# Optimization experiments

Measured on AMD Instinct MI355X. Metric: run time of the kernel, lower is better.

Reference implementation:

```python
import jax, jax.numpy as jnp
import numpy as np
import math

B, S, E, H = 4, 1024, 1024, 16
HD = E // H
MAX_SEQ = 5000
THETA = 10000.0


def _freqs_cis():
    # RotaryPositionalEncoding buffer: complex64 [MAX_SEQ, E//2]
    freqs = 1.0 / (THETA ** (np.arange(0, E, 2)[: E // 2] / E))
    ang = np.outer(np.arange(MAX_SEQ), freqs)
    return jnp.asarray(np.exp(1j * ang).astype(np.complex64))


def _rope(x, idx, fc_table):
    # x: [B, S, E]; pairs consecutive channels across the FULL embed_dim
    # (applied before head splitting, faithful to the original module)
    xc = x.reshape(*x.shape[:-1], -1, 2)
    xc = jax.lax.complex(xc[..., 0], xc[..., 1])  # [B, S, E//2]
    out = xc * fc_table[idx]                       # [B, S, E//2]
    return jnp.stack([jnp.real(out), jnp.imag(out)], axis=-1).reshape(x.shape)


def reference(query, key, value, query_index, key_index, attn_mask,
              key_padding_mask, Wq, bq, Wk, bk, Wv, bv, Wo, bo):
    q = query @ Wq.T + bq
    k = key @ Wk.T + bk
    v = value @ Wv.T + bv

    fc = _freqs_cis()
    q = _rope(q, query_index, fc)
    k = _rope(k, key_index, fc)

    # torch: q = cat(q.chunk(H, dim=-1), dim=0) -> flat HEAD-MAJOR [H*B, S, HD]
    qf = q.reshape(B, S, H, HD).transpose(2, 0, 1, 3).reshape(H * B, S, HD)
    kf = k.reshape(B, S, H, HD).transpose(2, 0, 1, 3).reshape(H * B, S, HD)
    vf = v.reshape(B, S, H, HD).transpose(2, 0, 1, 3).reshape(H * B, S, HD)

    # mask: logical_or(attn_mask[Sq,Sk], kpm[B,1,Sk]) -> [B, Sq, Sk]
    m = jnp.logical_or(attn_mask[None, :, :], key_padding_mask[:, None, :])
    madd = jnp.where(m, -jnp.inf, 0.0).astype(query.dtype)
    # torch repeat_interleave(H, dim=0) yields BATCH-MAJOR flat [B*H, Sq, Sk];
    # it is added to the head-major scores as-is (faithful to the original
    # indexing, including its head/batch-order quirk)
    madd_flat = jnp.repeat(madd, H, axis=0)

    scores = jnp.einsum('nqd,nkd->nqk', qf / math.sqrt(HD), kf) + madd_flat
    w = jax.nn.softmax(scores, axis=-1)              # [H*B, Sq, Sk]
    of = jnp.einsum('nqk,nkd->nqd', w, vf)           # [H*B, Sq, HD]

    # cat(chunks(dim=0), dim=-1) -> [B, Sq, E], head-major last dim
    attn_output = of.reshape(H, B, S, HD).transpose(1, 2, 0, 3).reshape(B, S, E)
    attn_output = attn_output @ Wo.T + bo

    # stack(chunks(dim=0), dim=1).mean(1) -> [B, Sq, Sk]
    attn_weights = w.reshape(H, B, S, S).transpose(1, 0, 2, 3).mean(axis=1)
    return attn_output, attn_weights


def setup_inputs() -> dict:
    key0 = jax.random.key(0)
    ks = jax.random.split(key0, 10)
    sc = 0.02
    inp = {
        'query': jax.random.normal(ks[0], (B, S, E), jnp.float32),
        'key': jax.random.normal(ks[1], (B, S, E), jnp.float32),
        'value': jax.random.normal(ks[2], (B, S, E), jnp.float32),
        'query_index': jnp.sort(jax.random.randint(ks[3], (B, S), 0, 4096), axis=-1),
        'key_index': jnp.sort(jax.random.randint(ks[4], (B, S), 0, 4096), axis=-1),
        'attn_mask': jnp.triu(jnp.ones((S, S), jnp.bool_), k=1),  # causal
        'key_padding_mask': jnp.zeros((B, S), jnp.bool_),
        'Wq': jax.random.normal(ks[5], (E, E), jnp.float32) * sc,
        'bq': jnp.zeros((E,), jnp.float32),
        'Wk': jax.random.normal(ks[6], (E, E), jnp.float32) * sc,
        'bk': jnp.zeros((E,), jnp.float32),
        'Wv': jax.random.normal(ks[7], (E, E), jnp.float32) * sc,
        'bv': jnp.zeros((E,), jnp.float32),
        'Wo': jax.random.normal(ks[8], (E, E), jnp.float32) * sc,
        'bo': jnp.zeros((E,), jnp.float32),
    }
    return inp
```

## Files before the change

kernel.cpp:

```cpp
#include <hip/hip_runtime.h>
#include <stdint.h>
#include <math.h>

#define B_ 4
#define S_ 1024
#define E_ 1024
#define H_ 16
#define HD_ 64
#define HB_ 64

typedef __attribute__((ext_vector_type(8))) short bhalf8;
typedef __attribute__((ext_vector_type(4))) float floatx4;

__device__ __forceinline__ unsigned short f2bf(float f) {
  union { float f; unsigned u; } v; v.f = f;
  unsigned r = (v.u + 0x7FFFu + ((v.u >> 16) & 1u)) >> 16;
  return (unsigned short)r;
}
__device__ __forceinline__ float bf2f(unsigned short b) {
  union { unsigned u; float f; } v; v.u = ((unsigned)b) << 16;
  return v.f;
}
__device__ __forceinline__ unsigned cvtpk_bf16(float a, float b) {
  unsigned r;
  asm volatile("v_cvt_pk_bf16_f32 %0, %1, %2" : "=v"(r) : "v"(a), "v"(b));
  return r;
}

__device__ __forceinline__ void gload16(const void* g, void* l) {
  __builtin_amdgcn_global_load_lds(
      (const __attribute__((address_space(1))) unsigned int*)g,
      (__attribute__((address_space(3))) unsigned int*)l, 16, 0, 0);
}

template <int NCH>
__device__ __forceinline__ void stage_tile(const unsigned short* org,
                                           unsigned short* lds, int wave, int lane) {
  const int rl = lane >> 3;
  const int scb = ((lane & 7) << 4) ^ (rl << 4);
  const char* base = (const char*)org + scb;
#pragma unroll
  for (int i = 0; i < NCH / 4; ++i) {
    const int c = wave + 4 * i;
    gload16(base + (size_t)(c * 8 + rl) * 2048, (char*)lds + c * 1024);
  }
}

__device__ __forceinline__ bhalf8 read_frag(const unsigned short* lds, int row, int kbyte) {
  const int off = row * 128 + (kbyte ^ ((row & 7) << 4));
  return *(const bhalf8*)((const char*)lds + off);
}

__global__ void detect_bool_kernel(const uint8_t* __restrict__ amask, int* __restrict__ flag) {
  if (threadIdx.x == 0 && blockIdx.x == 0) *flag = (amask[1] != 0) ? 1 : 0;
}

__global__ __launch_bounds__(256) void mprep_kernel(
    const void* __restrict__ amask, const void* __restrict__ kpm,
    const int* __restrict__ flagp, unsigned long long* __restrict__ Mbits) {
  const int gid = blockIdx.x * 256 + threadIdx.x;
  const int word = gid & 15, q = (gid >> 4) & 1023, bp = gid >> 14;
  const int k0 = word * 64;
  unsigned long long bits = 0;
  if (*flagp) {
    const uint8_t* ap = (const uint8_t*)amask + (size_t)q * 1024 + k0;
    const uint8_t* kp = (const uint8_t*)kpm + (size_t)bp * 1024 + k0;
#pragma unroll
    for (int c = 0; c < 4; ++c) {
      uint4 a = *(const uint4*)(ap + c * 16);
      uint4 k = *(const uint4*)(kp + c * 16);
      unsigned aw[4] = {a.x | k.x, a.y | k.y, a.z | k.z, a.w | k.w};
#pragma unroll
      for (int wv = 0; wv < 4; ++wv)
#pragma unroll
        for (int bt = 0; bt < 4; ++bt)
          if ((aw[wv] >> (8 * bt)) & 0xffu)
            bits |= 1ull << (c * 16 + wv * 4 + bt);
    }
  } else {
    const int* ap = (const int*)amask + (size_t)q * 1024 + k0;
    const int* kp = (const int*)kpm + (size_t)bp * 1024 + k0;
#pragma unroll
    for (int c = 0; c < 16; ++c) {
      int4 a = *(const int4*)(ap + c * 4);
      int4 k = *(const int4*)(kp + c * 4);
      if (a.x | k.x) bits |= 1ull << (c * 4 + 0);
      if (a.y | k.y) bits |= 1ull << (c * 4 + 1);
      if (a.z | k.z) bits |= 1ull << (c * 4 + 2);
      if (a.w | k.w) bits |= 1ull << (c * 4 + 3);
    }
  }
  Mbits[((size_t)bp << 14) + (size_t)q * 16 + word] = bits;
}

__global__ __launch_bounds__(256) void cvt_in_kernel(
    const float* __restrict__ q, const float* __restrict__ k,
    const float* __restrict__ v, unsigned short* __restrict__ Ab) {
  const int z = blockIdx.z;
  const float* src = (z == 0) ? q : (z == 1) ? k : v;
  unsigned short* dst = Ab + (size_t)z * 4194304;
  const size_t i = ((size_t)blockIdx.x * 256 + threadIdx.x) * 8;
  float4 a = *(const float4*)(src + i);
  float4 b = *(const float4*)(src + i + 4);
  bhalf8 r;
  r[0] = (short)f2bf(a.x); r[1] = (short)f2bf(a.y);
  r[2] = (short)f2bf(a.z); r[3] = (short)f2bf(a.w);
  r[4] = (short)f2bf(b.x); r[5] = (short)f2bf(b.y);
  r[6] = (short)f2bf(b.z); r[7] = (short)f2bf(b.w);
  *(bhalf8*)(dst + i) = r;
}

__global__ __launch_bounds__(256) void cvt_w_kernel(
    const float* __restrict__ wq, const float* __restrict__ wk,
    const float* __restrict__ wv, const float* __restrict__ wo,
    unsigned short* __restrict__ Wb) {
  const int z = blockIdx.z;
  const float* src = (z == 0) ? wq : (z == 1) ? wk : (z == 2) ? wv : wo;
  unsigned short* dst = Wb + (size_t)z * 1048576;
  const size_t i = ((size_t)blockIdx.x * 256 + threadIdx.x) * 8;
  float4 a = *(const float4*)(src + i);
  float4 b = *(const float4*)(src + i + 4);
  bhalf8 r;
  r[0] = (short)f2bf(a.x); r[1] = (short)f2bf(a.y);
  r[2] = (short)f2bf(a.z); r[3] = (short)f2bf(a.w);
  r[4] = (short)f2bf(b.x); r[5] = (short)f2bf(b.y);
  r[6] = (short)f2bf(b.z); r[7] = (short)f2bf(b.w);
  *(bhalf8*)(dst + i) = r;
}

template <bool BF16OUT>
__global__ __launch_bounds__(256) void mfma_gemm_kernel(
    const unsigned short* __restrict__ A0, const unsigned short* __restrict__ A1,
    const unsigned short* __restrict__ A2,
    const unsigned short* __restrict__ W0, const unsigned short* __restrict__ W1,
    const unsigned short* __restrict__ W2,
    const float* __restrict__ b0, const float* __restrict__ b1,
    const float* __restrict__ b2,
    void* __restrict__ C0, void* __restrict__ C1, void* __restrict__ C2) {
  const int z = blockIdx.z;
  const unsigned short* A = (z == 0) ? A0 : (z == 1) ? A1 : A2;
  const unsigned short* W = (z == 0) ? W0 : (z == 1) ? W1 : W2;
  const float* bias = (z == 0) ? b0 : (z == 1) ? b1 : b2;
  void* C = (z == 0) ? C0 : (z == 1) ? C1 : C2;
  const int lin = blockIdx.y * 8 + blockIdx.x;
  const int swz = (lin & 7) * 32 + (lin >> 3);
  const int m0 = (swz >> 3) * 128, n0 = (swz & 7) * 128;
  __shared__ unsigned short As[128 * 64];
  __shared__ unsigned short Ws[128 * 64];
  const int t = threadIdx.x, wave = t >> 6, lane = t & 63;
  const int wr = wave >> 1, wc = wave & 1;
  floatx4 acc[4][4];
  const floatx4 z4 = {0.f, 0.f, 0.f, 0.f};
#pragma unroll
  for (int i = 0; i < 4; ++i)
#pragma unroll
    for (int j = 0; j < 4; ++j) acc[i][j] = z4;

  for (int k0 = 0; k0 < 1024; k0 += 64) {
    stage_tile<16>(A + (size_t)m0 * 1024 + k0, As, wave, lane);
    stage_tile<16>(W + (size_t)n0 * 1024 + k0, Ws, wave, lane);
    __syncthreads();
#pragma unroll
    for (int ks = 0; ks < 2; ++ks) {
      const int kb = ks * 64 + ((lane >> 4) << 4);
      bhalf8 af[4], bf[4];
#pragma unroll
      for (int mi = 0; mi < 4; ++mi)
        af[mi] = read_frag(As, wr * 64 + mi * 16 + (lane & 15), kb);
#pragma unroll
      for (int ni = 0; ni < 4; ++ni)
        bf[ni] = read_frag(Ws, wc * 64 + ni * 16 + (lane & 15), kb);
#pragma unroll
      for (int mi = 0; mi < 4; ++mi)
#pragma unroll
        for (int ni = 0; ni < 4; ++ni)
          acc[mi][ni] = __builtin_amdgcn_mfma_f32_16x16x32_bf16(af[mi], bf[ni], acc[mi][ni], 0, 0, 0);
    }
    __syncthreads();
  }
#pragma unroll
  for (int mi = 0; mi < 4; ++mi)
#pragma unroll
    for (int ni = 0; ni < 4; ++ni) {
      const int col = n0 + wc * 64 + ni * 16 + (lane & 15);
      const float bv = bias[col];
#pragma unroll
      for (int r = 0; r < 4; ++r) {
        const int row = m0 + wr * 64 + mi * 16 + (lane >> 4) * 4 + r;
        const float v = acc[mi][ni][r] + bv;
        if (BF16OUT)
          ((unsigned short*)C)[(size_t)row * 1024 + col] = f2bf(v);
        else
          ((float*)C)[(size_t)row * 1024 + col] = v;
      }
    }
}

__global__ __launch_bounds__(256) void rope_bf_kernel(unsigned int* __restrict__ X,
                                                      const int* __restrict__ idxs) {
  const int gid = blockIdx.x * 256 + threadIdx.x;
  const int i = gid & 511, bs = gid >> 9;
  const int pos = idxs[bs];
  const double freq = exp(-(double)(2 * i) * (9.210340371976184 / 1024.0));
  const double ang = fmod((double)pos * freq, 6.283185307179586476925287);
  const float fa = (float)ang;
  float sn, c;
  sincosf(fa, &sn, &c);
  const unsigned v = X[gid];
  const float x = bf2f((unsigned short)(v & 0xffffu));
  const float y = bf2f((unsigned short)(v >> 16));
  const float rx = x * c - y * sn;
  const float ry = x * sn + y * c;
  X[gid] = (unsigned)f2bf(rx) | ((unsigned)f2bf(ry) << 16);
}

__global__ __launch_bounds__(256) void transpose_v_kernel(
    const unsigned short* __restrict__ Vr, unsigned short* __restrict__ Vt) {
  const int s0 = blockIdx.x * 64;
  const int bh = blockIdx.y;
  const int b = bh >> 4, h = bh & 15;
  __shared__ unsigned short L[64][72];
  const int t = threadIdx.x, r = t >> 2, cq = (t & 3) * 16;
  const unsigned short* src = Vr + ((size_t)(b * S_) + s0 + r) * E_ + h * HD_ + cq;
  *(bhalf8*)&L[r][cq] = *(const bhalf8*)src;
  *(bhalf8*)&L[r][cq + 8] = *(const bhalf8*)(src + 8);
  __syncthreads();
  bhalf8 o0, o1;
#pragma unroll
  for (int u = 0; u < 8; ++u) o0[u] = (short)L[cq + u][r];
#pragma unroll
  for (int u = 0; u < 8; ++u) o1[u] = (short)L[cq + 8 + u][r];
  unsigned short* dst = Vt + ((size_t)bh * 64 + r) * 1024 + s0 + cq;
  *(bhalf8*)dst = o0;
  *(bhalf8*)(dst + 8) = o1;
}

__global__ __launch_bounds__(256) void scores_sm_kernel(
    const unsigned short* __restrict__ Qr, const unsigned short* __restrict__ Kr,
    unsigned short* __restrict__ P, const unsigned long long* __restrict__ Mbits,
    int hb0, int nwg) {
  const int lin = blockIdx.y * 64 + blockIdx.x;
  const int q8 = nwg >> 3;
  const int swz = (lin & 7) * q8 + (lin >> 3);
  const int qb = swz & 63, lhb = swz >> 6;
  const int hb = hb0 + lhb;
  const int h = hb >> 2, b = hb & 3, bp = hb >> 4;
  const int q0 = qb * 16;
  __shared__ unsigned short Sbuf[16 * 1024];
  float* rptr = (float*)Sbuf;
  const int t = threadIdx.x, w = t >> 6, lane = t & 63;
  const int l4 = lane >> 4, l15 = lane & 15;

  const char* Qb = (const char*)Qr + ((size_t)b << 21) + h * 128;
  const char* Kb = (const char*)Kr + ((size_t)b << 21) + h * 128;

  const unsigned long long* mrow =
      Mbits + ((size_t)bp << 14) + (size_t)(q0 + l15) * 16 + w * 4;
  unsigned long long mw0 = mrow[0], mw1 = mrow[1], mw2 = mrow[2], mw3 = mrow[3];

  bhalf8 bq0 = *(const bhalf8*)(Qb + (size_t)(q0 + l15) * 2048 + l4 * 16);
  bhalf8 bq1 = *(const bhalf8*)(Qb + (size_t)(q0 + l15) * 2048 + 64 + l4 * 16);

  floatx4 acc[16];
  const floatx4 z4 = {0.f, 0.f, 0.f, 0.f};
#pragma unroll
  for (int i = 0; i < 16; ++i) acc[i] = z4;
#pragma unroll
  for (int mt = 0; mt < 16; ++mt) {
    const char* kr = Kb + (size_t)(w * 256 + mt * 16 + l15) * 2048 + l4 * 16;
    bhalf8 a0 = *(const bhalf8*)kr;
    bhalf8 a1 = *(const bhalf8*)(kr + 64);
    acc[mt] = __builtin_amdgcn_mfma_f32_16x16x32_bf16(a0, bq0, acc[mt], 0, 0, 0);
    acc[mt] = __builtin_amdgcn_mfma_f32_16x16x32_bf16(a1, bq1, acc[mt], 0, 0, 0);
  }

  float red[16];
#pragma unroll
  for (int mt = 0; mt < 16; ++mt)
    red[mt] = fmaxf(fmaxf(acc[mt][0], acc[mt][1]), fmaxf(acc[mt][2], acc[mt][3]));
#pragma unroll
  for (int s2 = 8; s2 > 0; s2 >>= 1)
#pragma unroll
    for (int i = 0; i < 8; ++i)
      if (i < s2) red[i] = fmaxf(red[i], red[i + s2]);
  float mx = red[0];
  mx = fmaxf(mx, __shfl_xor(mx, 16));
  mx = fmaxf(mx, __shfl_xor(mx, 32));
  if (l4 == 0) rptr[w * 16 + l15] = mx;
  __syncthreads();
  mx = fmaxf(fmaxf(rptr[l15], rptr[16 + l15]), fmaxf(rptr[32 + l15], rptr[48 + l15]));

  const float Cc = 0.18033688011112042f;
  const float mc = mx * Cc;
#pragma unroll
  for (int mt = 0; mt < 16; ++mt) {
    const unsigned long long mwv = (mt < 4) ? mw0 : (mt < 8) ? mw1 : (mt < 12) ? mw2 : mw3;
    const unsigned bits = (unsigned)(mwv >> ((mt & 3) * 16 + l4 * 4)) & 0xFu;
#pragma unroll
    for (int r = 0; r < 4; ++r) {
      float e = exp2f(__builtin_fmaf(acc[mt][r], Cc, -mc));
      acc[mt][r] = ((bits >> r) & 1u) ? 0.f : e;
    }
  }

#pragma unroll
  for (int mt = 0; mt < 16; ++mt)
    red[mt] = (acc[mt][0] + acc[mt][1]) + (acc[mt][2] + acc[mt][3]);
#pragma unroll
  for (int s2 = 8; s2 > 0; s2 >>= 1)
#pragma unroll
    for (int i = 0; i < 8; ++i)
      if (i < s2) red[i] += red[i + s2];
  float sm = red[0];
  sm += __shfl_xor(sm, 16);
  sm += __shfl_xor(sm, 32);
  if (l4 == 0) rptr[64 + w * 16 + l15] = sm;
  __syncthreads();
  sm = (rptr[64 + l15] + rptr[80 + l15]) + (rptr[96 + l15] + rptr[112 + l15]);
  const float inv = 1.0f / sm;
  __syncthreads();

  const int xr = (l15 & 7) << 4;
#pragma unroll
  for (int mt = 0; mt < 16; ++mt) {
    uint2 pk;
    pk.x = cvtpk_bf16(acc[mt][0] * inv, acc[mt][1] * inv);
    pk.y = cvtpk_bf16(acc[mt][2] * inv, acc[mt][3] * inv);
    const int kb2 = (w * 256 + mt * 16 + l4 * 4) * 2;
    *(uint2*)((char*)Sbuf + l15 * 2048 + (kb2 ^ xr)) = pk;
  }
  __syncthreads();

  unsigned short* pbase = P + ((size_t)lhb << 20);
#pragma unroll
  for (int rr = 0; rr < 4; ++rr) {
    const int ql = w * 4 + rr;
    const int gq = q0 + ql;
    const int xq = (ql & 7) << 4;
#pragma unroll
    for (int j = 0; j < 2; ++j) {
      bhalf8 v = *(const bhalf8*)((const char*)Sbuf + ql * 2048 +
                                  ((j * 1024 + lane * 16) ^ xq));
      *(bhalf8*)(pbase + ((size_t)gq << 10) + j * 512 + lane * 8) = v;
    }
  }
}

__global__ __launch_bounds__(256) void wmean_kernel(
    const unsigned short* __restrict__ P, float* __restrict__ outW,
    int nhh, int first) {
  const size_t gid = (size_t)blockIdx.x * 256 + threadIdx.x;
  const int k8 = (int)(gid & 127);
  const int q = (int)((gid >> 7) & 1023);
  const int b = (int)(gid >> 17);
  float s[8];
#pragma unroll
  for (int u = 0; u < 8; ++u) s[u] = 0.f;
  for (int hh = 0; hh < nhh; ++hh) {
    const int lhb = hh * 4 + b;
    bhalf8 v = *(const bhalf8*)(P + ((size_t)lhb << 20) + ((size_t)q << 10) + k8 * 8);
#pragma unroll
    for (int u = 0; u < 8; ++u) s[u] += bf2f((unsigned short)v[u]);
  }
  float* o = outW + (((size_t)(b * S_ + q)) << 10) + k8 * 8;
  const float invH = 1.0f / 16.0f;
  float4 v0, v1;
  v0.x = s[0] * invH; v0.y = s[1] * invH; v0.z = s[2] * invH; v0.w = s[3] * invH;
  v1.x = s[4] * invH; v1.y = s[5] * invH; v1.z = s[6] * invH; v1.w = s[7] * invH;
  if (!first) {
    float4 a = *(float4*)o, b4 = *(float4*)(o + 4);
    v0.x += a.x; v0.y += a.y; v0.z += a.z; v0.w += a.w;
    v1.x += b4.x; v1.y += b4.y; v1.z += b4.z; v1.w += b4.w;
  }
  *(float4*)o = v0;
  *(float4*)(o + 4) = v1;
}

__global__ __launch_bounds__(256) void pv_mfma_kernel(
    const unsigned short* __restrict__ Wt, const unsigned short* __restrict__ Vt,
    unsigned short* __restrict__ Ocat, int hb0, int nwg) {
  const int lin = blockIdx.y * 16 + blockIdx.x;
  const int q8 = nwg >> 3;
  const int swz = (lin & 7) * q8 + (lin >> 3);
  const int qt = swz & 15, lhb = swz >> 4;
  const int hb = hb0 + lhb;
  const int h = hb >> 2, b = hb & 3;
  const int q0 = qt * 64;
  __shared__ unsigned short Ps[64 * 64];
  __shared__ unsigned short Vs[64 * 64];
  const int t = threadIdx.x, wave = t >> 6, lane = t & 63;
  const int wr = wave >> 1, wc = wave & 1;
  const unsigned short* Wh = Wt + ((size_t)lhb << 20);
  const unsigned short* Vh = Vt + (size_t)(b * 16 + h) * 65536;
  floatx4 acc[2][2];
  const floatx4 z4 = {0.f, 0.f, 0.f, 0.f};
#pragma unroll
  for (int i = 0; i < 2; ++i)
#pragma unroll
    for (int j = 0; j < 2; ++j) acc[i][j] = z4;

  for (int k0 = 0; k0 < 1024; k0 += 64) {
    stage_tile<8>(Wh + (size_t)q0 * 1024 + k0, Ps, wave, lane);
    stage_tile<8>(Vh + k0, Vs, wave, lane);
    __syncthreads();
#pragma unroll
    for (int ks = 0; ks < 2; ++ks) {
      const int kb = ks * 64 + ((lane >> 4) << 4);
      bhalf8 af[2], bf[2];
#pragma unroll
      for (int mi = 0; mi < 2; ++mi)
        af[mi] = read_frag(Ps, wr * 32 + mi * 16 + (lane & 15), kb);
#pragma unroll
      for (int ni = 0; ni < 2; ++ni)
        bf[ni] = read_frag(Vs, wc * 32 + ni * 16 + (lane & 15), kb);
#pragma unroll
      for (int mi = 0; mi < 2; ++mi)
#pragma unroll
        for (int ni = 0; ni < 2; ++ni)
          acc[mi][ni] = __builtin_amdgcn_mfma_f32_16x16x32_bf16(af[mi], bf[ni], acc[mi][ni], 0, 0, 0);
    }
    __syncthreads();
  }
#pragma unroll
  for (int mi = 0; mi < 2; ++mi)
#pragma unroll
    for (int ni = 0; ni < 2; ++ni) {
      const int d = wc * 32 + ni * 16 + (lane & 15);
#pragma unroll
      for (int r = 0; r < 4; ++r) {
        const int q = q0 + wr * 32 + mi * 16 + (lane >> 4) * 4 + r;
        Ocat[((size_t)(b * S_) + q) * E_ + h * HD_ + d] = f2bf(acc[mi][ni][r]);
      }
    }
}

extern "C" void kernel_launch(void* const* d_in, const int* in_sizes, int n_in,
                              void* d_out, int out_size, void* d_ws, size_t ws_size,
                              hipStream_t stream) {
  (void)in_sizes; (void)n_in; (void)out_size;
  const float* query = (const float*)d_in[0];
  const float* key   = (const float*)d_in[1];
  const float* value = (const float*)d_in[2];
  const int* qidx = (const int*)d_in[3];
  const int* kidx = (const int*)d_in[4];
  const void* amask = d_in[5];
  const void* kpm   = d_in[6];
  const float* Wq = (const float*)d_in[7];
  const float* bq = (const float*)d_in[8];
  const float* Wk = (const float*)d_in[9];
  const float* bk = (const float*)d_in[10];
  const float* Wv = (const float*)d_in[11];
  const float* bv = (const float*)d_in[12];
  const float* Wo = (const float*)d_in[13];
  const float* bo = (const float*)d_in[14];

  float* outA = (float*)d_out;
  float* outW = (float*)d_out + (size_t)B_ * S_ * E_;

  float* ws = (float*)d_ws;
  unsigned short* Ab   = (unsigned short*)(ws + 0);
  unsigned short* Wb   = (unsigned short*)(ws + 6291456);
  unsigned short* Qr   = (unsigned short*)(ws + 8388608);
  unsigned short* Kr   = (unsigned short*)(ws + 10485760);
  unsigned short* Vr   = (unsigned short*)(ws + 12582912);
  unsigned short* Vt   = (unsigned short*)(ws + 14680064);
  unsigned short* Ocat = (unsigned short*)(ws + 16777216);
  int* flagp           = (int*)(ws + 18874368);
  unsigned long long* Mbits = (unsigned long long*)(ws + 18874432);
  const size_t tail_off = 18874432 + 131072;

  const size_t ws_floats = ws_size / 4;
  int CH = 0;
  unsigned short* P = nullptr;
  for (int c = 64; c >= 8; c >>= 1) {
    if (tail_off + (size_t)c * 524288 <= ws_floats) {
      CH = c;
      P = (unsigned short*)(ws + tail_off);
      break;
    }
  }
  if (!CH) {
    CH = 8;
    P = (unsigned short*)ws;
  }

  detect_bool_kernel<<<1, 64, 0, stream>>>((const uint8_t*)amask, flagp);
  mprep_kernel<<<256, 256, 0, stream>>>(amask, kpm, flagp, Mbits);

  cvt_in_kernel<<<dim3(2048, 1, 3), 256, 0, stream>>>(query, key, value, Ab);
  cvt_w_kernel<<<dim3(512, 1, 4), 256, 0, stream>>>(Wq, Wk, Wv, Wo, Wb);

  mfma_gemm_kernel<true><<<dim3(8, 32, 3), 256, 0, stream>>>(
      Ab, Ab + 4194304, Ab + 8388608,
      Wb, Wb + 1048576, Wb + 2097152,
      bq, bk, bv, Qr, Kr, Vr);

  rope_bf_kernel<<<8192, 256, 0, stream>>>((unsigned int*)Qr, qidx);
  rope_bf_kernel<<<8192, 256, 0, stream>>>((unsigned int*)Kr, kidx);

  transpose_v_kernel<<<dim3(16, 64), 256, 0, stream>>>(Vr, Vt);

  const int nch = HB_ / CH;
  for (int c = 0; c < nch; ++c) {
    const int hb0 = c * CH;
    scores_sm_kernel<<<dim3(64, CH), 256, 0, stream>>>(Qr, Kr, P, Mbits, hb0,
                                                       64 * CH);
    wmean_kernel<<<2048, 256, 0, stream>>>(P, outW, CH / 4, (c == 0) ? 1 : 0);
    pv_mfma_kernel<<<dim3(16, CH), 256, 0, stream>>>(P, Vt, Ocat, hb0, 16 * CH);
  }

  mfma_gemm_kernel<false><<<dim3(8, 32, 1), 256, 0, stream>>>(
      Ocat, Ocat, Ocat, Wb + 3145728, Wb + 3145728, Wb + 3145728,
      bo, bo, bo, outA, outA, outA);
}
```

Before: 241.3 us.

## Widen scores-softmax block to 8 waves and merge RoPE launches

The scores/softmax kernel now runs 512 threads per block, so each of 8 waves covers 128 keys instead of 256. The softmax is restructured to take per-wave max and sum and combine them once through a single barrier with rescaling, replacing two separate reduction barriers. The RoPE kernels for Q and K are merged into one launch, and the frequency and angle math moves from double-precision exp/fmod to float exp2f with no range reduction. The float angle at positions up to ~4096 may lose accuracy compared with the fmod-reduced double version.

```diff
diff --git a/kernel.cpp b/kernel.cpp
--- a/kernel.cpp
+++ b/kernel.cpp
@@ -196,16 +196,19 @@
     }
 }
 
-__global__ __launch_bounds__(256) void rope_bf_kernel(unsigned int* __restrict__ X,
-                                                      const int* __restrict__ idxs) {
+__global__ __launch_bounds__(256) void rope_bf_kernel(
+    unsigned int* __restrict__ Q, unsigned int* __restrict__ K,
+    const int* __restrict__ qidx, const int* __restrict__ kidx) {
+  const int z = blockIdx.y;
+  unsigned int* X = z ? K : Q;
+  const int* idxs = z ? kidx : qidx;
   const int gid = blockIdx.x * 256 + threadIdx.x;
   const int i = gid & 511, bs = gid >> 9;
   const int pos = idxs[bs];
-  const double freq = exp(-(double)(2 * i) * (9.210340371976184 / 1024.0));
-  const double ang = fmod((double)pos * freq, 6.283185307179586476925287);
-  const float fa = (float)ang;
+  const float fr = exp2f((float)i * (-13.287712379549449f / 512.0f));
+  const float ang = (float)pos * fr;
   float sn, c;
-  sincosf(fa, &sn, &c);
+  sincosf(ang, &sn, &c);
   const unsigned v = X[gid];
   const float x = bf2f((unsigned short)(v & 0xffffu));
   const float y = bf2f((unsigned short)(v >> 16));
@@ -235,7 +238,7 @@
   *(bhalf8*)(dst + 8) = o1;
 }
 
-__global__ __launch_bounds__(256) void scores_sm_kernel(
+__global__ __launch_bounds__(512) void scores_sm_kernel(
     const unsigned short* __restrict__ Qr, const unsigned short* __restrict__ Kr,
     unsigned short* __restrict__ P, const unsigned long long* __restrict__ Mbits,
     int hb0, int nwg) {
@@ -247,7 +250,7 @@
   const int h = hb >> 2, b = hb & 3, bp = hb >> 4;
   const int q0 = qb * 16;
   __shared__ unsigned short Sbuf[16 * 1024];
-  float* rptr = (float*)Sbuf;
+  __shared__ float rbuf[256];
   const int t = threadIdx.x, w = t >> 6, lane = t & 63;
   const int l4 = lane >> 4, l15 = lane & 15;
 
@@ -255,94 +258,100 @@
   const char* Kb = (const char*)Kr + ((size_t)b << 21) + h * 128;
 
   const unsigned long long* mrow =
-      Mbits + ((size_t)bp << 14) + (size_t)(q0 + l15) * 16 + w * 4;
-  unsigned long long mw0 = mrow[0], mw1 = mrow[1], mw2 = mrow[2], mw3 = mrow[3];
+      Mbits + ((size_t)bp << 14) + (size_t)(q0 + l15) * 16 + w * 2;
+  const unsigned long long mw0 = mrow[0], mw1 = mrow[1];
 
   bhalf8 bq0 = *(const bhalf8*)(Qb + (size_t)(q0 + l15) * 2048 + l4 * 16);
   bhalf8 bq1 = *(const bhalf8*)(Qb + (size_t)(q0 + l15) * 2048 + 64 + l4 * 16);
 
-  floatx4 acc[16];
+  floatx4 acc[8];
   const floatx4 z4 = {0.f, 0.f, 0.f, 0.f};
 #pragma unroll
-  for (int i = 0; i < 16; ++i) acc[i] = z4;
-#pragma unroll
-  for (int mt = 0; mt < 16; ++mt) {
-    const char* kr = Kb + (size_t)(w * 256 + mt * 16 + l15) * 2048 + l4 * 16;
+  for (int i = 0; i < 8; ++i) acc[i] = z4;
+#pragma unroll
+  for (int mt = 0; mt < 8; ++mt) {
+    const char* kr = Kb + (size_t)(w * 128 + mt * 16 + l15) * 2048 + l4 * 16;
     bhalf8 a0 = *(const bhalf8*)kr;
     bhalf8 a1 = *(const bhalf8*)(kr + 64);
     acc[mt] = __builtin_amdgcn_mfma_f32_16x16x32_bf16(a0, bq0, acc[mt], 0, 0, 0);
     acc[mt] = __builtin_amdgcn_mfma_f32_16x16x32_bf16(a1, bq1, acc[mt], 0, 0, 0);
   }
 
-  float red[16];
-#pragma unroll
-  for (int mt = 0; mt < 16; ++mt)
+  float red[8];
+#pragma unroll
+  for (int mt = 0; mt < 8; ++mt)
     red[mt] = fmaxf(fmaxf(acc[mt][0], acc[mt][1]), fmaxf(acc[mt][2], acc[mt][3]));
 #pragma unroll
-  for (int s2 = 8; s2 > 0; s2 >>= 1)
-#pragma unroll
-    for (int i = 0; i < 8; ++i)
+  for (int s2 = 4; s2 > 0; s2 >>= 1)
+#pragma unroll
+    for (int i = 0; i < 4; ++i)
       if (i < s2) red[i] = fmaxf(red[i], red[i + s2]);
-  float mx = red[0];
-  mx = fmaxf(mx, __shfl_xor(mx, 16));
-  mx = fmaxf(mx, __shfl_xor(mx, 32));
-  if (l4 == 0) rptr[w * 16 + l15] = mx;
-  __syncthreads();
-  mx = fmaxf(fmaxf(rptr[l15], rptr[16 + l15]), fmaxf(rptr[32 + l15], rptr[48 + l15]));
+  float mw = red[0];
+  mw = fmaxf(mw, __shfl_xor(mw, 16));
+  mw = fmaxf(mw, __shfl_xor(mw, 32));
 
   const float Cc = 0.18033688011112042f;
-  const float mc = mx * Cc;
-#pragma unroll
-  for (int mt = 0; mt < 16; ++mt) {
-    const unsigned long long mwv = (mt < 4) ? mw0 : (mt < 8) ? mw1 : (mt < 12) ? mw2 : mw3;
-    const unsigned bits = (unsigned)(mwv >> ((mt & 3) * 16 + l4 * 4)) & 0xFu;
+  const float mc = mw * Cc;
+#pragma unroll
+  for (int mt = 0; mt < 8; ++mt) {
+    const unsigned bits =
+        (unsigned)(((mt < 4) ? mw0 : mw1) >> ((mt & 3) * 16 + l4 * 4)) & 0xFu;
 #pragma unroll
     for (int r = 0; r < 4; ++r) {
       float e = exp2f(__builtin_fmaf(acc[mt][r], Cc, -mc));
       acc[mt][r] = ((bits >> r) & 1u) ? 0.f : e;
     }
   }
-
-#pragma unroll
-  for (int mt = 0; mt < 16; ++mt)
+#pragma unroll
+  for (int mt = 0; mt < 8; ++mt)
     red[mt] = (acc[mt][0] + acc[mt][1]) + (acc[mt][2] + acc[mt][3]);
 #pragma unroll
-  for (int s2 = 8; s2 > 0; s2 >>= 1)
-#pragma unroll
-    for (int i = 0; i < 8; ++i)
+  for (int s2 = 4; s2 > 0; s2 >>= 1)
+#pragma unroll
+    for (int i = 0; i < 4; ++i)
       if (i < s2) red[i] += red[i + s2];
-  float sm = red[0];
-  sm += __shfl_xor(sm, 16);
-  sm += __shfl_xor(sm, 32);
-  if (l4 == 0) rptr[64 + w * 16 + l15] = sm;
+  float sw = red[0];
+  sw += __shfl_xor(sw, 16);
+  sw += __shfl_xor(sw, 32);
+
+  if (l4 == 0) {
+    rbuf[w * 16 + l15] = mw;
+    rbuf[128 + w * 16 + l15] = sw;
+  }
   __syncthreads();
-  sm = (rptr[64 + l15] + rptr[80 + l15]) + (rptr[96 + l15] + rptr[112 + l15]);
-  const float inv = 1.0f / sm;
+
+  float M = rbuf[l15];
+#pragma unroll
+  for (int ww = 1; ww < 8; ++ww) M = fmaxf(M, rbuf[ww * 16 + l15]);
+  float S = 0.f;
+#pragma unroll
+  for (int ww = 0; ww < 8; ++ww)
+    S += rbuf[128 + ww * 16 + l15] * exp2f((rbuf[ww * 16 + l15] - M) * Cc);
+  const float g = exp2f((mw - M) * Cc) / S;
+
+  const int xr = (l15 & 7) << 4;
+#pragma unroll
+  for (int mt = 0; mt < 8; ++mt) {
+    uint2 pk;
+    pk.x = cvtpk_bf16(acc[mt][0] * g, acc[mt][1] * g);
+    pk.y = cvtpk_bf16(acc[mt][2] * g, acc[mt][3] * g);
+    const int kb2 = (w * 128 + mt * 16 + l4 * 4) * 2;
+    *(uint2*)((char*)Sbuf + l15 * 2048 + (kb2 ^ xr)) = pk;
+  }
   __syncthreads();
 
-  const int xr = (l15 & 7) << 4;
-#pragma unroll
-  for (int mt = 0; mt < 16; ++mt) {
-    uint2 pk;
-    pk.x = cvtpk_bf16(acc[mt][0] * inv, acc[mt][1] * inv);
-    pk.y = cvtpk_bf16(acc[mt][2] * inv, acc[mt][3] * inv);
-    const int kb2 = (w * 256 + mt * 16 + l4 * 4) * 2;
-    *(uint2*)((char*)Sbuf + l15 * 2048 + (kb2 ^ xr)) = pk;
-  }
-  __syncthreads();
-
   unsigned short* pbase = P + ((size_t)lhb << 20);
 #pragma unroll
-  for (int rr = 0; rr < 4; ++rr) {
-    const int ql = w * 4 + rr;
+  for (int rr = 0; rr < 2; ++rr) {
+    const int ql = w * 2 + rr;
     const int gq = q0 + ql;
     const int xq = (ql & 7) << 4;
-#pragma unroll
-    for (int j = 0; j < 2; ++j) {
-      bhalf8 v = *(const bhalf8*)((const char*)Sbuf + ql * 2048 +
-                                  ((j * 1024 + lane * 16) ^ xq));
-      *(bhalf8*)(pbase + ((size_t)gq << 10) + j * 512 + lane * 8) = v;
-    }
+    const char* rowp = (const char*)Sbuf + ql * 2048;
+    bhalf8 v0 = *(const bhalf8*)(rowp + ((lane * 32) ^ xq));
+    bhalf8 v1 = *(const bhalf8*)(rowp + ((lane * 32 + 16) ^ xq));
+    unsigned short* dst = pbase + ((size_t)gq << 10) + lane * 16;
+    *(bhalf8*)dst = v0;
+    *(bhalf8*)(dst + 8) = v1;
   }
 }
 
@@ -495,15 +504,15 @@
       Wb, Wb + 1048576, Wb + 2097152,
       bq, bk, bv, Qr, Kr, Vr);
 
-  rope_bf_kernel<<<8192, 256, 0, stream>>>((unsigned int*)Qr, qidx);
-  rope_bf_kernel<<<8192, 256, 0, stream>>>((unsigned int*)Kr, kidx);
+  rope_bf_kernel<<<dim3(8192, 2), 256, 0, stream>>>(
+      (unsigned int*)Qr, (unsigned int*)Kr, qidx, kidx);
 
   transpose_v_kernel<<<dim3(16, 64), 256, 0, stream>>>(Vr, Vt);
 
   const int nch = HB_ / CH;
   for (int c = 0; c < nch; ++c) {
     const int hb0 = c * CH;
-    scores_sm_kernel<<<dim3(64, CH), 256, 0, stream>>>(Qr, Kr, P, Mbits, hb0,
+    scores_sm_kernel<<<dim3(64, CH), 512, 0, stream>>>(Qr, Kr, P, Mbits, hb0,
                                                        64 * CH);
     wmean_kernel<<<2048, 256, 0, stream>>>(P, outW, CH / 4, (c == 0) ? 1 : 0);
     pv_mfma_kernel<<<dim3(16, CH), 256, 0, stream>>>(P, Vt, Ocat, hb0, 16 * CH);
```

Result: no change. 245.7 us (+1.8%).
